# Optimization experiments

Measured on AMD Instinct MI355X. Metric: run time of the kernel, lower is better.

Reference implementation:

```python
import jax, jax.numpy as jnp
import numpy as np
from jax import lax

H = 512          # gru_dim
E = 512          # embed_dim
N_MELS = 80
EPS = 1e-5


def setup_inputs() -> dict:
    key = jax.random.key(0)
    ks = list(jax.random.split(key, 20))

    def w(k, shape):
        fan_in = int(np.prod(shape[:-1]))
        return (jax.random.normal(k, shape, jnp.float32) / np.sqrt(fan_in)).astype(jnp.float32)

    inp = {}
    inp["x"] = jax.random.randint(ks[0], (8, 8192), 0, 256, dtype=jnp.int32)
    inp["mel"] = jax.random.normal(ks[1], (8, 40, N_MELS), jnp.float32)
    inp["embed_w"] = jax.random.normal(ks[2], (256, E), jnp.float32) * 0.02
    # UpsampleNetwork convs (WIO kernels)
    inp["conv_in_w"] = w(ks[3], (3, N_MELS, 512)); inp["conv_in_b"] = jnp.zeros((512,), jnp.float32)
    inp["conv_d1_w"] = w(ks[4], (2, 512, 512));    inp["conv_d1_b"] = jnp.zeros((512,), jnp.float32)
    inp["conv_d2_w"] = w(ks[5], (2, 512, 512));    inp["conv_d2_b"] = jnp.zeros((512,), jnp.float32)
    inp["up1_w"] = w(ks[6], (1, 512, 512)); inp["up1_b"] = jnp.zeros((512,), jnp.float32)
    inp["up2_w"] = w(ks[7], (1, 512, 512)); inp["up2_b"] = jnp.zeros((512,), jnp.float32)
    inp["up3_w"] = w(ks[8], (1, 512, E));   inp["up3_b"] = jnp.zeros((E,), jnp.float32)
    for name, c in [("bn_in", 512), ("bn_d1", 512), ("bn_d2", 512), ("bn_u1", 512), ("bn_u2", 512), ("bn_u3", E)]:
        inp[name + "_s"] = jnp.ones((c,), jnp.float32)
        inp[name + "_o"] = jnp.zeros((c,), jnp.float32)
    # GRU params (haiku layout: w_i [E,3H], w_h [H,3H], b [3H]; order z,r,a)
    inp["gru_wi"] = w(ks[9], (E, 3 * H))
    inp["gru_wh"] = w(ks[10], (H, 3 * H))
    inp["gru_b"] = jnp.zeros((3 * H,), jnp.float32)
    inp["o1_w"] = w(ks[11], (H, H)); inp["o1_b"] = jnp.zeros((H,), jnp.float32)
    inp["o2_w"] = w(ks[12], (H, 256)); inp["o2_b"] = jnp.zeros((256,), jnp.float32)
    return inp


def _bn(h, s, o):
    # haiku BatchNorm training-mode: stats over all but channel axis
    m = jnp.mean(h, axis=(0, 1))
    v = jnp.mean(jnp.square(h), axis=(0, 1)) - m * m
    return (h - m) * (s * lax.rsqrt(v + EPS)) + o


def _conv(h, w, b, rate=1):
    return lax.conv_general_dilated(h, w, (1,), 'VALID', rhs_dilation=(rate,),
                                    dimension_numbers=('NWC', 'WIO', 'NWC')) + b


def _tconv(h, w, b, stride):
    return lax.conv_transpose(h, w, (stride,), 'SAME',
                              dimension_numbers=('NWC', 'WIO', 'NWC')) + b


def _upsample(mel, conv_in_w, conv_in_b, bn_in_s, bn_in_o,
              conv_d1_w, conv_d1_b, bn_d1_s, bn_d1_o,
              conv_d2_w, conv_d2_b, bn_d2_s, bn_d2_o,
              up1_w, up1_b, bn_u1_s, bn_u1_o,
              up2_w, up2_b, bn_u2_s, bn_u2_o,
              up3_w, up3_b, bn_u3_s, bn_u3_o):
    u = jax.nn.relu(_bn(_conv(mel, conv_in_w, conv_in_b), bn_in_s, bn_in_o))
    r1 = jax.nn.relu(_bn(_conv(u, conv_d1_w, conv_d1_b, rate=2), bn_d1_s, bn_d1_o))
    u = u[:, 1:-1] + r1
    r2 = jax.nn.relu(_bn(_conv(u, conv_d2_w, conv_d2_b, rate=4), bn_d2_s, bn_d2_o))
    u = u[:, 2:-2] + r2
    u = jax.nn.relu(_bn(_tconv(u, up1_w, up1_b, 2), bn_u1_s, bn_u1_o))
    u = jax.nn.relu(_bn(_tconv(u, up2_w, up2_b, 2), bn_u2_s, bn_u2_o))
    u = jax.nn.relu(_bn(_tconv(u, up3_w, up3_b, 4), bn_u3_s, bn_u3_o))
    N, L, D = u.shape
    u = jnp.tile(u[:, :, None, :], (1, 1, 16, 1))
    return jnp.reshape(u, (N, L * 16, D))


def reference(x, mel, embed_w,
              conv_in_w, conv_in_b, bn_in_s, bn_in_o,
              conv_d1_w, conv_d1_b, bn_d1_s, bn_d1_o,
              conv_d2_w, conv_d2_b, bn_d2_s, bn_d2_o,
              up1_w, up1_b, bn_u1_s, bn_u1_o,
              up2_w, up2_b, bn_u2_s, bn_u2_o,
              up3_w, up3_b, bn_u3_s, bn_u3_o,
              gru_wi, gru_wh, gru_b, o1_w, o1_b, o2_w, o2_b):
    cond = _upsample(mel, conv_in_w, conv_in_b, bn_in_s, bn_in_o,
                     conv_d1_w, conv_d1_b, bn_d1_s, bn_d1_o,
                     conv_d2_w, conv_d2_b, bn_d2_s, bn_d2_o,
                     up1_w, up1_b, bn_u1_s, bn_u1_o,
                     up2_w, up2_b, bn_u2_s, bn_u2_o,
                     up3_w, up3_b, bn_u3_s, bn_u3_o)
    inp = embed_w[x] + cond  # [N, L, E]
    N = inp.shape[0]
    # precompute input contribution to all gates as one big matmul, time-major
    gx = jnp.einsum('nle,ek->lnk', inp, gru_wi)  # [L, N, 3H]
    wh_zr, wh_a = gru_wh[:, :2 * H], gru_wh[:, 2 * H:]
    b_zr, b_a = gru_b[:2 * H], gru_b[2 * H:]

    def step(h, g):
        zr = jax.nn.sigmoid(g[:, :2 * H] + h @ wh_zr + b_zr)
        z, r = jnp.split(zr, 2, axis=-1)
        a = jnp.tanh(g[:, 2 * H:] + (r * h) @ wh_a + b_a)
        hn = (1.0 - z) * h + z * a
        return hn, hn

    h0 = jnp.zeros((N, H), inp.dtype)
    _, ys = lax.scan(step, h0, gx)           # [L, N, H]
    hseq = jnp.transpose(ys, (1, 0, 2))       # [N, L, H]
    logits = jax.nn.relu(hseq @ o1_w + o1_b) @ o2_w + o2_b
    return jax.nn.log_softmax(logits, axis=-1)
```

## Files before the change

### kernel.cpp

```cpp
#include <hip/hip_runtime.h>

#define EPSV 1e-5f

#define AT_LD(p)    __hip_atomic_load((p), __ATOMIC_RELAXED, __HIP_MEMORY_SCOPE_AGENT)
#define AT_ST(p, v) __hip_atomic_store((p), (v), __ATOMIC_RELAXED, __HIP_MEMORY_SCOPE_AGENT)

static constexpr long OFF_FRH   = 0;
static constexpr long OFF_FH    = 8192;
static constexpr long OFF_SRH   = 16384;
static constexpr long OFF_SH    = 24576;
static constexpr long OFF_BAR   = 32768;
static constexpr long OFF_MEAN  = 33280;
static constexpr long OFF_SCALE = 33792;
static constexpr long OFF_OFFS  = 34304;
static constexpr long OFF_U0    = 40960;
static constexpr long OFF_U0N   = OFF_U0    + 155648;
static constexpr long OFF_R1    = OFF_U0N   + 155648;
static constexpr long OFF_U1    = OFF_R1    + 147456;
static constexpr long OFF_R2    = OFF_U1    + 147456;
static constexpr long OFF_U2    = OFF_R2    + 131072;
static constexpr long OFF_Y1    = OFF_U2    + 131072;
static constexpr long OFF_V1    = OFF_Y1    + 262144;
static constexpr long OFF_Y2    = OFF_V1    + 262144;
static constexpr long OFF_V2    = OFF_Y2    + 524288;
static constexpr long OFF_Y3    = OFF_V2    + 524288;
static constexpr long OFF_COND0 = OFF_Y3    + 2097152;
static constexpr long OFF_EWI   = OFF_COND0 + 2097152;
static constexpr long OFF_CGX   = OFF_EWI   + 393216;
static constexpr long OFF_HSEQ  = OFF_CGX   + 6291456;

__global__ void init_kernel(unsigned long long* tagbase, unsigned* bar) {
    int t = blockIdx.x * 256 + threadIdx.x;
    if (t < 16384) AT_ST(&tagbase[t], 0ull);
    if (t == 0) AT_ST(bar, 0u);
}

__global__ void conv1d_kernel(const float* __restrict__ in, const float* __restrict__ w,
                              const float* __restrict__ b, float* __restrict__ out,
                              int T_in, int T_out, int Cin, int K, int rate) {
    extern __shared__ float s_in[];
    int n = blockIdx.x / T_out, t = blockIdx.x % T_out;
    int Cout = blockDim.x;
    for (int idx = threadIdx.x; idx < K * Cin; idx += Cout) {
        int k = idx / Cin, i = idx - k * Cin;
        s_in[idx] = in[((long)(n * T_in + t + k * rate)) * Cin + i];
    }
    __syncthreads();
    int c = threadIdx.x;
    float acc = b[c];
    for (int j = 0; j < K * Cin; ++j)
        acc += s_in[j] * w[(long)j * Cout + c];
    out[((long)(n * T_out + t)) * Cout + c] = acc;
}

__global__ void tconv1d_kernel(const float* __restrict__ in, const float* __restrict__ w,
                               const float* __restrict__ b, float* __restrict__ out,
                               int T_in, int stride, int Cin) {
    extern __shared__ float s_in[];
    int T_out = T_in * stride;
    int n = blockIdx.x / T_out, s = blockIdx.x % T_out;
    int Cout = blockDim.x;
    int c = threadIdx.x;
    if (s % stride) { out[((long)(n * T_out + s)) * Cout + c] = b[c]; return; }
    for (int i = threadIdx.x; i < Cin; i += Cout)
        s_in[i] = in[((long)(n * T_in + s / stride)) * Cin + i];
    __syncthreads();
    float acc = b[c];
    for (int i = 0; i < Cin; ++i) acc += s_in[i] * w[(long)i * Cout + c];
    out[((long)(n * T_out + s)) * Cout + c] = acc;
}

__global__ void bnstats_kernel(const float* __restrict__ x, const float* __restrict__ bns,
                               const float* __restrict__ bno, float* mean, float* scale,
                               float* offs, int count, int C) {
    int c = blockIdx.x, t = threadIdx.x;
    float s = 0.f, s2 = 0.f;
    for (int j = t; j < count; j += 64) { float v = x[(long)j * C + c]; s += v; s2 += v * v; }
    for (int off = 32; off; off >>= 1) { s += __shfl_down(s, off); s2 += __shfl_down(s2, off); }
    if (t == 0) {
        float m = s / count;
        float var = s2 / count - m * m;
        mean[c] = m;
        scale[c] = bns[c] * rsqrtf(var + EPSV);
        offs[c] = bno[c];
    }
}

__global__ void bnapply_kernel(const float* __restrict__ x, float* __restrict__ out,
                               const float* mean, const float* scale, const float* offs,
                               long total) {
    long i = (long)blockIdx.x * 256 + threadIdx.x;
    if (i >= total) return;
    int c = (int)(i & 511);
    float v = (x[i] - mean[c]) * scale[c] + offs[c];
    out[i] = fmaxf(v, 0.f);
}

__global__ void bnapply_add_kernel(const float* __restrict__ r, const float* __restrict__ base,
                                   float* __restrict__ out, const float* mean, const float* scale,
                                   const float* offs, int T_out, int T_base, int shift) {
    long i = (long)blockIdx.x * 256 + threadIdx.x;
    long total = (long)8 * T_out * 512;
    if (i >= total) return;
    int c = (int)(i & 511);
    long row = i >> 9;
    int n = (int)(row / T_out), t = (int)(row % T_out);
    float v = (r[i] - mean[c]) * scale[c] + offs[c];
    v = fmaxf(v, 0.f);
    out[i] = base[(((long)(n * T_base + t + shift)) << 9) + c] + v;
}

__global__ void __launch_bounds__(256) rowgemm_kernel(const float* __restrict__ A,
                                                      const float* __restrict__ W,
                                                      float* __restrict__ out, int rows) {
    __shared__ float sA[16 * 512];
    long r0 = (long)blockIdx.x * 16;
    int t = threadIdx.x;
    for (int idx = t; idx < 16 * 512; idx += 256) sA[idx] = A[r0 * 512 + idx];
    __syncthreads();
    float acc[16][6];
#pragma unroll
    for (int r = 0; r < 16; ++r)
#pragma unroll
        for (int j = 0; j < 6; ++j) acc[r][j] = 0.f;
    for (int e = 0; e < 512; ++e) {
        float wv[6];
#pragma unroll
        for (int j = 0; j < 6; ++j) wv[j] = W[(long)e * 1536 + t + 256 * j];
#pragma unroll
        for (int r = 0; r < 16; ++r) {
            float a = sA[r * 512 + e];
#pragma unroll
            for (int j = 0; j < 6; ++j) acc[r][j] += a * wv[j];
        }
    }
    for (int r = 0; r < 16; ++r)
#pragma unroll
        for (int j = 0; j < 6; ++j) out[(r0 + r) * 1536 + t + 256 * j] = acc[r][j];
}

#define GRU_SMEM_FLOATS (3 * 16 * 520 + 512 + 512 + 48)

__device__ __forceinline__ unsigned long long fast_ld(const unsigned long long* p) {
    unsigned long long v;
    asm volatile("global_load_dwordx2 %0, %1, off sc0\n\ts_waitcnt vmcnt(0)"
                 : "=&v"(v) : "v"(p) : "memory");
    return v;
}

__device__ __forceinline__ void pub_word(unsigned long long* fp, unsigned long long* sp,
                                         unsigned ep, float val) {
    unsigned long long w = ((unsigned long long)ep << 32) | (unsigned long long)__float_as_uint(val);
    *fp = w;
    AT_ST(sp, w);
}

__device__ __forceinline__ float wait_word(const unsigned long long* fp,
                                           const unsigned long long* sp,
                                           unsigned ep, int& fails) {
    if (fails < 4) {
#pragma unroll 1
        for (int k = 0; k < 8; ++k) {
            unsigned long long v = fast_ld(fp);
            if ((unsigned)(v >> 32) >= ep)
                return __uint_as_float((unsigned)(v & 0xFFFFFFFFull));
        }
        ++fails;
    }
    unsigned long long v = AT_LD(sp);
    while ((unsigned)(v >> 32) < ep) {
        __builtin_amdgcn_s_sleep(1);
        v = AT_LD(sp);
    }
    return __uint_as_float((unsigned)(v & 0xFFFFFFFFull));
}

__global__ void __launch_bounds__(512, 1) gru_kernel(
    const float* __restrict__ wh, const float* __restrict__ gb, const int* __restrict__ x,
    const float* __restrict__ ewi, const float* __restrict__ cgx,
    unsigned long long* __restrict__ fRH, unsigned long long* __restrict__ fH,
    unsigned long long* __restrict__ sRH, unsigned long long* __restrict__ sH,
    unsigned* __restrict__ bar, float* __restrict__ hseq) {
    extern __shared__ float sm[];
    float* Wzt = sm;
    float* Wrt = Wzt + 16 * 520;
    float* Wat = Wrt + 16 * 520;
    float* h_l = Wat + 16 * 520;
    float* rh_l = h_l + 512;
    float* bz = rh_l + 512;
    float* br = bz + 16;
    float* ba = br + 16;

    int wg = blockIdx.x;
    int n = wg & 7;
    int role = wg >> 3;
    int base = role * 16;
    int t = threadIdx.x;

    unsigned long long* fRHn = fRH + n * 512;
    unsigned long long* fHn = fH + n * 512;
    unsigned long long* sRHn = sRH + n * 512;
    unsigned long long* sHn = sH + n * 512;

    for (int idx = t; idx < 512 * 16; idx += 512) {
        int i = idx >> 4, c = idx & 15;
        Wzt[c * 520 + i] = wh[(long)i * 1536 + base + c];
        Wrt[c * 520 + i] = wh[(long)i * 1536 + 512 + base + c];
        Wat[c * 520 + i] = wh[(long)i * 1536 + 1024 + base + c];
    }
    if (t < 16) { bz[t] = gb[base + t]; br[t] = gb[512 + base + t]; ba[t] = gb[1024 + base + t]; }
    h_l[t] = 0.f;

    bool own = ((t >> 4) == role);
    fRHn[t] = 0ull;
    fHn[t] = 0ull;
    if (own) { AT_ST(&sRHn[t], 0ull); AT_ST(&sHn[t], 0ull); }
    asm volatile("s_waitcnt vmcnt(0)" ::: "memory");
    __syncthreads();
    if (t == 0) {
        __hip_atomic_fetch_add(bar, 1u, __ATOMIC_RELAXED, __HIP_MEMORY_SCOPE_AGENT);
        for (int it = 0; it < 20000000; ++it) {
            if (AT_LD(bar) >= 256u) break;
            __builtin_amdgcn_s_sleep(2);
        }
    }
    __syncthreads();

    const float* cgxn = cgx + (long)n * 512 * 1536;
    int col = t >> 5, sub = t & 31;
    const float* Wz_c = Wzt + col * 520;
    const float* Wr_c = Wrt + col * 520;
    const float* Wa_c = Wat + col * 520;

    int fails = 0;

    float gz = 0.f, gr = 0.f, ga = 0.f;
    if (sub == 0) {
        int xv = x[n * 8192];
        const float* e_row = ewi + (long)xv * 1536;
        gz = e_row[base + col] + cgxn[base + col] + bz[col];
        gr = e_row[512 + base + col] + cgxn[512 + base + col] + br[col];
        ga = e_row[1024 + base + col] + cgxn[1024 + base + col] + ba[col];
    }

    for (int l = 0; l < 8192; ++l) {
        unsigned ep = (unsigned)(l + 1);

        float accr = 0.f;
#pragma unroll
        for (int k = 0; k < 16; ++k) {
            int i = sub + (k << 5);
            accr += h_l[i] * Wr_c[i];
        }
        accr += __shfl_down(accr, 16, 32);
        accr += __shfl_down(accr, 8, 32);
        accr += __shfl_down(accr, 4, 32);
        accr += __shfl_down(accr, 2, 32);
        accr += __shfl_down(accr, 1, 32);
        if (sub == 0) {
            float rr = 1.f / (1.f + __expf(-(gr + accr)));
            float rhv = rr * h_l[base + col];
            rh_l[base + col] = rhv;
            pub_word(&fRHn[base + col], &sRHn[base + col], ep, rhv);
        }

        float accz = 0.f;
#pragma unroll
        for (int k = 0; k < 16; ++k) {
            int i = sub + (k << 5);
            accz += h_l[i] * Wz_c[i];
        }
        accz += __shfl_down(accz, 16, 32);
        accz += __shfl_down(accz, 8, 32);
        accz += __shfl_down(accz, 4, 32);
        accz += __shfl_down(accz, 2, 32);
        accz += __shfl_down(accz, 1, 32);
        float z = (sub == 0) ? 1.f / (1.f + __expf(-(gz + accz))) : 0.f;

        if (!own) rh_l[t] = wait_word(&fRHn[t], &sRHn[t], ep, fails);
        __syncthreads();

        float acca = 0.f;
#pragma unroll
        for (int k = 0; k < 16; ++k) {
            int i = sub + (k << 5);
            acca += rh_l[i] * Wa_c[i];
        }
        acca += __shfl_down(acca, 16, 32);
        acca += __shfl_down(acca, 8, 32);
        acca += __shfl_down(acca, 4, 32);
        acca += __shfl_down(acca, 2, 32);
        acca += __shfl_down(acca, 1, 32);
        if (sub == 0) {
            float pre = ga + acca;
            float axv = fabsf(pre);
            float ex = __expf(-2.f * axv);
            float th = (1.f - ex) / (1.f + ex);
            float a = copysignf(th, pre);
            float hn = (1.f - z) * h_l[base + col] + z * a;
            h_l[base + col] = hn;
            if (l != 8191) pub_word(&fHn[base + col], &sHn[base + col], ep, hn);
            hseq[(((long)n * 8192 + l) << 9) + base + col] = hn;
        }
        if (l == 8191) break;

        if (sub == 0) {
            int xv = x[n * 8192 + l + 1];
            const float* e_row = ewi + (long)xv * 1536;
            const float* c_row = cgxn + (long)((l + 1) >> 4) * 1536;
            gz = e_row[base + col] + c_row[base + col] + bz[col];
            gr = e_row[512 + base + col] + c_row[512 + base + col] + br[col];
            ga = e_row[1024 + base + col] + c_row[1024 + base + col] + ba[col];
        }

        if (!own) h_l[t] = wait_word(&fHn[t], &sHn[t], ep, fails);
        __syncthreads();
    }
}

__global__ void __launch_bounds__(256) head_kernel(const float* __restrict__ hseq,
                                                   const float* __restrict__ o1w,
                                                   const float* __restrict__ o1b,
                                                   const float* __restrict__ o2w,
                                                   const float* __restrict__ o2b,
                                                   float* __restrict__ out) {
    __shared__ float hs[16 * 512];
    long row0 = (long)blockIdx.x * 16;
    int t = threadIdx.x;
    for (int idx = t; idx < 16 * 512; idx += 256) hs[idx] = hseq[row0 * 512 + idx];
    __syncthreads();

    int c0 = t, c1 = t + 256;
    float acc[16][2];
#pragma unroll
    for (int r = 0; r < 16; ++r) { acc[r][0] = o1b[c0]; acc[r][1] = o1b[c1]; }
    for (int i = 0; i < 512; ++i) {
        float w0 = o1w[(long)i * 512 + c0], w1 = o1w[(long)i * 512 + c1];
#pragma unroll
        for (int r = 0; r < 16; ++r) {
            float h = hs[r * 512 + i];
            acc[r][0] += h * w0;
            acc[r][1] += h * w1;
        }
    }
    __syncthreads();
#pragma unroll
    for (int r = 0; r < 16; ++r) {
        hs[r * 512 + c0] = fmaxf(acc[r][0], 0.f);
        hs[r * 512 + c1] = fmaxf(acc[r][1], 0.f);
    }
    __syncthreads();

    float acc2[16];
#pragma unroll
    for (int r = 0; r < 16; ++r) acc2[r] = o2b[t];
    for (int i = 0; i < 512; ++i) {
        float w = o2w[(long)i * 256 + t];
#pragma unroll
        for (int r = 0; r < 16; ++r) acc2[r] += hs[r * 512 + i] * w;
    }
    __syncthreads();
#pragma unroll
    for (int r = 0; r < 16; ++r) hs[r * 256 + t] = acc2[r];
    __syncthreads();

    int wave = t >> 6, lane = t & 63;
    for (int rr = 0; rr < 4; ++rr) {
        int r = wave * 4 + rr;
        float v0 = hs[r * 256 + lane];
        float v1 = hs[r * 256 + 64 + lane];
        float v2 = hs[r * 256 + 128 + lane];
        float v3 = hs[r * 256 + 192 + lane];
        float m = fmaxf(fmaxf(v0, v1), fmaxf(v2, v3));
        for (int off = 32; off; off >>= 1) m = fmaxf(m, __shfl_xor(m, off));
        float s = __expf(v0 - m) + __expf(v1 - m) + __expf(v2 - m) + __expf(v3 - m);
        for (int off = 32; off; off >>= 1) s += __shfl_xor(s, off);
        float ls = m + logf(s);
        long ob = (row0 + r) * 256;
        out[ob + lane] = v0 - ls;
        out[ob + 64 + lane] = v1 - ls;
        out[ob + 128 + lane] = v2 - ls;
        out[ob + 192 + lane] = v3 - ls;
    }
}

extern "C" void kernel_launch(void* const* d_in, const int* in_sizes, int n_in,
                              void* d_out, int out_size, void* d_ws, size_t ws_size,
                              hipStream_t stream) {
    const int* x = (const int*)d_in[0];
    const float* mel = (const float*)d_in[1];
    const float* embed_w = (const float*)d_in[2];
    const float* conv_in_w = (const float*)d_in[3];
    const float* conv_in_b = (const float*)d_in[4];
    const float* conv_d1_w = (const float*)d_in[5];
    const float* conv_d1_b = (const float*)d_in[6];
    const float* conv_d2_w = (const float*)d_in[7];
    const float* conv_d2_b = (const float*)d_in[8];
    const float* up1_w = (const float*)d_in[9];
    const float* up1_b = (const float*)d_in[10];
    const float* up2_w = (const float*)d_in[11];
    const float* up2_b = (const float*)d_in[12];
    const float* up3_w = (const float*)d_in[13];
    const float* up3_b = (const float*)d_in[14];
    const float* bn_in_s = (const float*)d_in[15];
    const float* bn_in_o = (const float*)d_in[16];
    const float* bn_d1_s = (const float*)d_in[17];
    const float* bn_d1_o = (const float*)d_in[18];
    const float* bn_d2_s = (const float*)d_in[19];
    const float* bn_d2_o = (const float*)d_in[20];
    const float* bn_u1_s = (const float*)d_in[21];
    const float* bn_u1_o = (const float*)d_in[22];
    const float* bn_u2_s = (const float*)d_in[23];
    const float* bn_u2_o = (const float*)d_in[24];
    const float* bn_u3_s = (const float*)d_in[25];
    const float* bn_u3_o = (const float*)d_in[26];
    const float* gru_wi = (const float*)d_in[27];
    const float* gru_wh = (const float*)d_in[28];
    const float* gru_b = (const float*)d_in[29];
    const float* o1_w = (const float*)d_in[30];
    const float* o1_b = (const float*)d_in[31];
    const float* o2_w = (const float*)d_in[32];
    const float* o2_b = (const float*)d_in[33];

    float* ws = (float*)d_ws;
    float* out = (float*)d_out;

    unsigned long long* fRH = (unsigned long long*)(ws + OFF_FRH);
    unsigned long long* fH  = (unsigned long long*)(ws + OFF_FH);
    unsigned long long* sRH = (unsigned long long*)(ws + OFF_SRH);
    unsigned long long* sH  = (unsigned long long*)(ws + OFF_SH);
    unsigned* bar = (unsigned*)(ws + OFF_BAR);
    float* mean = ws + OFF_MEAN;
    float* scale = ws + OFF_SCALE;
    float* offs = ws + OFF_OFFS;
    float* u0 = ws + OFF_U0;
    float* u0n = ws + OFF_U0N;
    float* r1 = ws + OFF_R1;
    float* u1 = ws + OFF_U1;
    float* r2 = ws + OFF_R2;
    float* u2 = ws + OFF_U2;
    float* y1 = ws + OFF_Y1;
    float* v1 = ws + OFF_V1;
    float* y2 = ws + OFF_Y2;
    float* v2 = ws + OFF_V2;
    float* y3 = ws + OFF_Y3;
    float* cond0 = ws + OFF_COND0;
    float* ewi = ws + OFF_EWI;
    float* cgx = ws + OFF_CGX;
    float* hseq = ws + OFF_HSEQ;

    init_kernel<<<64, 256, 0, stream>>>(fRH, bar);

    conv1d_kernel<<<8 * 38, 512, 240 * 4, stream>>>(mel, conv_in_w, conv_in_b, u0, 40, 38, 80, 3, 1);
    bnstats_kernel<<<512, 64, 0, stream>>>(u0, bn_in_s, bn_in_o, mean, scale, offs, 304, 512);
    bnapply_kernel<<<155648 / 256, 256, 0, stream>>>(u0, u0n, mean, scale, offs, 155648);
    conv1d_kernel<<<8 * 36, 512, 1024 * 4, stream>>>(u0n, conv_d1_w, conv_d1_b, r1, 38, 36, 512, 2, 2);
    bnstats_kernel<<<512, 64, 0, stream>>>(r1, bn_d1_s, bn_d1_o, mean, scale, offs, 288, 512);
    bnapply_add_kernel<<<147456 / 256, 256, 0, stream>>>(r1, u0n, u1, mean, scale, offs, 36, 38, 1);
    conv1d_kernel<<<8 * 32, 512, 1024 * 4, stream>>>(u1, conv_d2_w, conv_d2_b, r2, 36, 32, 512, 2, 4);
    bnstats_kernel<<<512, 64, 0, stream>>>(r2, bn_d2_s, bn_d2_o, mean, scale, offs, 256, 512);
    bnapply_add_kernel<<<131072 / 256, 256, 0, stream>>>(r2, u1, u2, mean, scale, offs, 32, 36, 2);
    tconv1d_kernel<<<8 * 64, 512, 2048, stream>>>(u2, up1_w, up1_b, y1, 32, 2, 512);
    bnstats_kernel<<<512, 64, 0, stream>>>(y1, bn_u1_s, bn_u1_o, mean, scale, offs, 512, 512);
    bnapply_kernel<<<262144 / 256, 256, 0, stream>>>(y1, v1, mean, scale, offs, 262144);
    tconv1d_kernel<<<8 * 128, 512, 2048, stream>>>(v1, up2_w, up2_b, y2, 64, 2, 512);
    bnstats_kernel<<<512, 64, 0, stream>>>(y2, bn_u2_s, bn_u2_o, mean, scale, offs, 1024, 512);
    bnapply_kernel<<<524288 / 256, 256, 0, stream>>>(y2, v2, mean, scale, offs, 524288);
    tconv1d_kernel<<<8 * 512, 512, 2048, stream>>>(v2, up3_w, up3_b, y3, 128, 4, 512);
    bnstats_kernel<<<512, 64, 0, stream>>>(y3, bn_u3_s, bn_u3_o, mean, scale, offs, 4096, 512);
    bnapply_kernel<<<2097152 / 256, 256, 0, stream>>>(y3, cond0, mean, scale, offs, 2097152);

    rowgemm_kernel<<<16, 256, 0, stream>>>(embed_w, gru_wi, ewi, 256);
    rowgemm_kernel<<<256, 256, 0, stream>>>(cond0, gru_wi, cgx, 4096);

    hipFuncSetAttribute(reinterpret_cast<const void*>(gru_kernel),
                        hipFuncAttributeMaxDynamicSharedMemorySize,
                        (int)(GRU_SMEM_FLOATS * sizeof(float)));
    gru_kernel<<<256, 512, GRU_SMEM_FLOATS * sizeof(float), stream>>>(
        gru_wh, gru_b, x, ewi, cgx, fRH, fH, sRH, sH, bar, hseq);

    head_kernel<<<4096, 256, 0, stream>>>(hseq, o1_w, o1_b, o2_w, o2_b, out);
}
```

Measured before the change: 23.91 ms.

## Keep GRU recurrent weights in registers and restructure per-step exchange

Each thread now holds its 16-element slices of the z, r and a recurrent weight columns in registers instead of reading transposed copies from LDS every step. Each step reads the hidden state through a padded, swizzled LDS buffer as float4 loads, and the z and r dot products are fused into one loop with interleaved shuffle reductions. All threads now wait on the published h and r*h words, including their own, and the loop is reordered so the h-wait starts each step. The aim is to cut LDS traffic and latency on the serial recurrence critical path, at the cost of more registers and an extra global wait per own element.

Measured after the change: 41.54 ms. 73.7% more time.

```diff
diff --git a/kernel.cpp b/kernel.cpp
--- a/kernel.cpp
+++ b/kernel.cpp
@@ -139,7 +139,7 @@
         for (int j = 0; j < 6; ++j) out[(r0 + r) * 1536 + t + 256 * j] = acc[r][j];
 }
 
-#define GRU_SMEM_FLOATS (3 * 16 * 520 + 512 + 512 + 48)
+#define GRU_LDS_BYTES 86016
 
 __device__ __forceinline__ unsigned long long fast_ld(const unsigned long long* p) {
     unsigned long long v;
@@ -182,39 +182,36 @@
     unsigned long long* __restrict__ sRH, unsigned long long* __restrict__ sH,
     unsigned* __restrict__ bar, float* __restrict__ hseq) {
     extern __shared__ float sm[];
-    float* Wzt = sm;
-    float* Wrt = Wzt + 16 * 520;
-    float* Wat = Wrt + 16 * 520;
-    float* h_l = Wat + 16 * 520;
-    float* rh_l = h_l + 512;
-    float* bz = rh_l + 512;
-    float* br = bz + 16;
-    float* ba = br + 16;
+    float* h_sw = sm;
+    float* rh_sw = sm + 640;
 
     int wg = blockIdx.x;
     int n = wg & 7;
     int role = wg >> 3;
     int base = role * 16;
     int t = threadIdx.x;
+    int col = t >> 5, sub = t & 31;
+    bool lead = (sub == 0);
 
     unsigned long long* fRHn = fRH + n * 512;
     unsigned long long* fHn = fH + n * 512;
     unsigned long long* sRHn = sRH + n * 512;
     unsigned long long* sHn = sH + n * 512;
 
-    for (int idx = t; idx < 512 * 16; idx += 512) {
-        int i = idx >> 4, c = idx & 15;
-        Wzt[c * 520 + i] = wh[(long)i * 1536 + base + c];
-        Wrt[c * 520 + i] = wh[(long)i * 1536 + 512 + base + c];
-        Wat[c * 520 + i] = wh[(long)i * 1536 + 1024 + base + c];
-    }
-    if (t < 16) { bz[t] = gb[base + t]; br[t] = gb[512 + base + t]; ba[t] = gb[1024 + base + t]; }
-    h_l[t] = 0.f;
-
-    bool own = ((t >> 4) == role);
+    float Wz[16], Wr[16], Wa[16];
+#pragma unroll
+    for (int k = 0; k < 16; ++k) {
+        long row = (long)(sub * 16 + k) * 1536;
+        Wz[k] = wh[row + base + col];
+        Wr[k] = wh[row + 512 + base + col];
+        Wa[k] = wh[row + 1024 + base + col];
+    }
+    float bzv = 0.f, brv = 0.f, bav = 0.f;
+    if (lead) { bzv = gb[base + col]; brv = gb[512 + base + col]; bav = gb[1024 + base + col]; }
+
+    fHn[t] = 0ull;
     fRHn[t] = 0ull;
-    fHn[t] = 0ull;
-    if (own) { AT_ST(&sRHn[t], 0ull); AT_ST(&sHn[t], 0ull); }
+    if ((t >> 4) == role) { AT_ST(&sRHn[t], 0ull); AT_ST(&sHn[t], 0ull); }
     asm volatile("s_waitcnt vmcnt(0)" ::: "memory");
     __syncthreads();
     if (t == 0) {
@@ -227,94 +224,101 @@
     __syncthreads();
 
     const float* cgxn = cgx + (long)n * 512 * 1536;
-    int col = t >> 5, sub = t & 31;
-    const float* Wz_c = Wzt + col * 520;
-    const float* Wr_c = Wrt + col * 520;
-    const float* Wa_c = Wat + col * 520;
-
+    int swz = (t >> 4) * 20 + (t & 15);
     int fails = 0;
+    float h_own = 0.f;
 
     float gz = 0.f, gr = 0.f, ga = 0.f;
-    if (sub == 0) {
+    if (lead) {
         int xv = x[n * 8192];
         const float* e_row = ewi + (long)xv * 1536;
-        gz = e_row[base + col] + cgxn[base + col] + bz[col];
-        gr = e_row[512 + base + col] + cgxn[512 + base + col] + br[col];
-        ga = e_row[1024 + base + col] + cgxn[1024 + base + col] + ba[col];
+        gz = e_row[base + col] + cgxn[base + col] + bzv;
+        gr = e_row[512 + base + col] + cgxn[512 + base + col] + brv;
+        ga = e_row[1024 + base + col] + cgxn[1024 + base + col] + bav;
     }
 
     for (int l = 0; l < 8192; ++l) {
         unsigned ep = (unsigned)(l + 1);
 
-        float accr = 0.f;
+        float hw = (l == 0) ? 0.f : wait_word(&fHn[t], &sHn[t], (unsigned)l, fails);
+        h_sw[swz] = hw;
+        __syncthreads();
+
+        float hb[16];
+        {
+            const float4* hp = (const float4*)(h_sw + sub * 20);
+            float4 q0 = hp[0], q1 = hp[1], q2 = hp[2], q3 = hp[3];
+            hb[0]=q0.x; hb[1]=q0.y; hb[2]=q0.z; hb[3]=q0.w;
+            hb[4]=q1.x; hb[5]=q1.y; hb[6]=q1.z; hb[7]=q1.w;
+            hb[8]=q2.x; hb[9]=q2.y; hb[10]=q2.z; hb[11]=q2.w;
+            hb[12]=q3.x; hb[13]=q3.y; hb[14]=q3.z; hb[15]=q3.w;
+        }
+
+        float accr = 0.f, accz = 0.f;
 #pragma unroll
         for (int k = 0; k < 16; ++k) {
-            int i = sub + (k << 5);
-            accr += h_l[i] * Wr_c[i];
+            accr += hb[k] * Wr[k];
+            accz += hb[k] * Wz[k];
         }
         accr += __shfl_down(accr, 16, 32);
+        accz += __shfl_down(accz, 16, 32);
         accr += __shfl_down(accr, 8, 32);
+        accz += __shfl_down(accz, 8, 32);
         accr += __shfl_down(accr, 4, 32);
+        accz += __shfl_down(accz, 4, 32);
         accr += __shfl_down(accr, 2, 32);
+        accz += __shfl_down(accz, 2, 32);
         accr += __shfl_down(accr, 1, 32);
-        if (sub == 0) {
+        accz += __shfl_down(accz, 1, 32);
+        float z = 0.f;
+        if (lead) {
             float rr = 1.f / (1.f + __expf(-(gr + accr)));
-            float rhv = rr * h_l[base + col];
-            rh_l[base + col] = rhv;
+            float rhv = rr * h_own;
             pub_word(&fRHn[base + col], &sRHn[base + col], ep, rhv);
-        }
-
-        float accz = 0.f;
-#pragma unroll
-        for (int k = 0; k < 16; ++k) {
-            int i = sub + (k << 5);
-            accz += h_l[i] * Wz_c[i];
-        }
-        accz += __shfl_down(accz, 16, 32);
-        accz += __shfl_down(accz, 8, 32);
-        accz += __shfl_down(accz, 4, 32);
-        accz += __shfl_down(accz, 2, 32);
-        accz += __shfl_down(accz, 1, 32);
-        float z = (sub == 0) ? 1.f / (1.f + __expf(-(gz + accz))) : 0.f;
-
-        if (!own) rh_l[t] = wait_word(&fRHn[t], &sRHn[t], ep, fails);
+            z = 1.f / (1.f + __expf(-(gz + accz)));
+        }
+
+        float rhw = wait_word(&fRHn[t], &sRHn[t], ep, fails);
+        rh_sw[swz] = rhw;
         __syncthreads();
 
+        float rb[16];
+        {
+            const float4* rp = (const float4*)(rh_sw + sub * 20);
+            float4 q0 = rp[0], q1 = rp[1], q2 = rp[2], q3 = rp[3];
+            rb[0]=q0.x; rb[1]=q0.y; rb[2]=q0.z; rb[3]=q0.w;
+            rb[4]=q1.x; rb[5]=q1.y; rb[6]=q1.z; rb[7]=q1.w;
+            rb[8]=q2.x; rb[9]=q2.y; rb[10]=q2.z; rb[11]=q2.w;
+            rb[12]=q3.x; rb[13]=q3.y; rb[14]=q3.z; rb[15]=q3.w;
+        }
+
         float acca = 0.f;
 #pragma unroll
-        for (int k = 0; k < 16; ++k) {
-            int i = sub + (k << 5);
-            acca += rh_l[i] * Wa_c[i];
-        }
+        for (int k = 0; k < 16; ++k) acca += rb[k] * Wa[k];
         acca += __shfl_down(acca, 16, 32);
         acca += __shfl_down(acca, 8, 32);
         acca += __shfl_down(acca, 4, 32);
         acca += __shfl_down(acca, 2, 32);
         acca += __shfl_down(acca, 1, 32);
-        if (sub == 0) {
+        if (lead) {
             float pre = ga + acca;
             float axv = fabsf(pre);
             float ex = __expf(-2.f * axv);
             float th = (1.f - ex) / (1.f + ex);
             float a = copysignf(th, pre);
-            float hn = (1.f - z) * h_l[base + col] + z * a;
-            h_l[base + col] = hn;
+            float hn = (1.f - z) * h_own + z * a;
+            h_own = hn;
             if (l != 8191) pub_word(&fHn[base + col], &sHn[base + col], ep, hn);
             hseq[(((long)n * 8192 + l) << 9) + base + col] = hn;
-        }
-        if (l == 8191) break;
-
-        if (sub == 0) {
-            int xv = x[n * 8192 + l + 1];
-            const float* e_row = ewi + (long)xv * 1536;
-            const float* c_row = cgxn + (long)((l + 1) >> 4) * 1536;
-            gz = e_row[base + col] + c_row[base + col] + bz[col];
-            gr = e_row[512 + base + col] + c_row[512 + base + col] + br[col];
-            ga = e_row[1024 + base + col] + c_row[1024 + base + col] + ba[col];
-        }
-
-        if (!own) h_l[t] = wait_word(&fHn[t], &sHn[t], ep, fails);
-        __syncthreads();
+            if (l != 8191) {
+                int xv = x[n * 8192 + l + 1];
+                const float* e_row = ewi + (long)xv * 1536;
+                const float* c_row = cgxn + (long)((l + 1) >> 4) * 1536;
+                gz = e_row[base + col] + c_row[base + col] + bzv;
+                gr = e_row[512 + base + col] + c_row[512 + base + col] + brv;
+                ga = e_row[1024 + base + col] + c_row[1024 + base + col] + bav;
+            }
+        }
     }
 }
 
@@ -475,8 +479,8 @@
 
     hipFuncSetAttribute(reinterpret_cast<const void*>(gru_kernel),
                         hipFuncAttributeMaxDynamicSharedMemorySize,
-                        (int)(GRU_SMEM_FLOATS * sizeof(float)));
-    gru_kernel<<<256, 512, GRU_SMEM_FLOATS * sizeof(float), stream>>>(
+                        GRU_LDS_BYTES);
+    gru_kernel<<<256, 512, GRU_LDS_BYTES, stream>>>(
         gru_wh, gru_b, x, ewi, cgx, fRH, fH, sRH, sH, bar, hseq);
 
     head_kernel<<<4096, 256, 0, stream>>>(hseq, o1_w, o1_b, o2_w, o2_b, out);
```
